# Optimization experiments

Measured on AMD Instinct MI355X. Metric: run time of the kernel, lower is better.

The kernel has to match this reference:

```python
import jax, jax.numpy as jnp
import numpy as np

D_MODEL = 1024
D_STATE = 16
BATCH = 16384
LN_EPS = 1e-5


def _linear_params(key, out_d, in_d):
    # torch nn.Linear default init: U(-1/sqrt(in_d), 1/sqrt(in_d))
    bound = 1.0 / np.sqrt(in_d)
    kw, kb = jax.random.split(key)
    W = jax.random.uniform(kw, (out_d, in_d), minval=-bound, maxval=bound, dtype=jnp.float32)
    b = jax.random.uniform(kb, (out_d,), minval=-bound, maxval=bound, dtype=jnp.float32)
    return W, b


def setup_inputs() -> dict:
    key = jax.random.key(0)
    k_x, k_b, k_c, k_dt, k_o = jax.random.split(key, 5)
    Wb, bb = _linear_params(k_b, D_STATE, D_MODEL)
    Wc, bc = _linear_params(k_c, D_STATE, D_MODEL)
    Wdt, bdt = _linear_params(k_dt, D_MODEL, D_MODEL)
    Wo, bo = _linear_params(k_o, D_MODEL, D_MODEL)
    return {
        "x": jax.random.normal(k_x, (BATCH, D_MODEL), dtype=jnp.float32),
        "gamma": jnp.ones((D_MODEL,), jnp.float32),   # LayerNorm weight
        "beta": jnp.zeros((D_MODEL,), jnp.float32),   # LayerNorm bias
        "Wb": Wb, "bb": bb,
        "Wc": Wc, "bc": bc,
        "Wdt": Wdt, "bdt": bdt,
        "D_skip": jnp.ones((D_MODEL,), jnp.float32),  # self.D parameter
        "Wo": Wo, "bo": bo,
    }


def reference(x, gamma, beta, Wb, bb, Wc, bc, Wdt, bdt, D_skip, Wo, bo):
    residual = x
    # LayerNorm
    mu = jnp.mean(x, axis=-1, keepdims=True)
    var = jnp.var(x, axis=-1, keepdims=True)
    xn = (x - mu) * jax.lax.rsqrt(var + LN_EPS) * gamma + beta  # (B, D)

    Bm = xn @ Wb.T + bb                     # (B, N)
    Cm = xn @ Wc.T + bc                     # (B, N)
    dt = jax.nn.softplus(xn @ Wdt.T + bdt)  # (B, D)
    # dA = exp(dt[...,None] * -exp(A_log)) is computed in the original but unused.

    # h = dt[:,:,None] * Bm[:,None,:] * xn[:,:,None]; y = (h * Cm[:,None,:]).sum(-1)
    # The N-reduction factors: sum_n Bm[b,n]*Cm[b,n] is d-independent.
    s = jnp.sum(Bm * Cm, axis=-1, keepdims=True)  # (B, 1)
    y = dt * xn * s + xn * D_skip                 # (B, D)

    y = y @ Wo.T + bo
    return y + residual  # dropout is identity at inference
```

## Files before the change

kernel.cpp:

```cpp
#include <hip/hip_runtime.h>
#include <math.h>

#define BATCH   16384
#define DMODEL  1024
#define NSTATE  16
#define LN_EPS  1e-5f

typedef __bf16 bf16x8 __attribute__((ext_vector_type(8)));
typedef float  f32x4  __attribute__((ext_vector_type(4)));

static __device__ __forceinline__ unsigned short f2bf(float v) {
  union { float f; unsigned u; } c; c.f = v;
  unsigned r = c.u + 0x7fffu + ((c.u >> 16) & 1u);
  return (unsigned short)(r >> 16);
}
static __device__ __forceinline__ float bf2f(unsigned short h) {
  union { unsigned u; float f; } c; c.u = ((unsigned)h) << 16;
  return c.f;
}

static __device__ __forceinline__ void gload16(const void* g, void* l) {
  __builtin_amdgcn_global_load_lds(
      (const __attribute__((address_space(1))) void*)g,
      (__attribute__((address_space(3))) void*)l, 16, 0, 0);
}

__global__ __launch_bounds__(256) void split_kernel(
    const float* __restrict__ src, unsigned short* __restrict__ hi,
    unsigned short* __restrict__ lo, int n) {
  int i = blockIdx.x * 256 + threadIdx.x;
  if (i < n) {
    float v = src[i];
    unsigned short h = f2bf(v);
    hi[i] = h;
    lo[i] = f2bf(v - bf2f(h));
  }
}

__global__ __launch_bounds__(256) void ln_kernel(
    const float* __restrict__ x, const float* __restrict__ gamma,
    const float* __restrict__ beta, unsigned short* __restrict__ xnh,
    unsigned short* __restrict__ xnl) {
  const int row = blockIdx.x;
  const int tid = threadIdx.x;
  const float4* xr = (const float4*)(x + (size_t)row * DMODEL);
  float4 v = xr[tid];
  float s = v.x + v.y + v.z + v.w;
  float q = v.x * v.x + v.y * v.y + v.z * v.z + v.w * v.w;
#pragma unroll
  for (int m = 1; m < 64; m <<= 1) {
    s += __shfl_xor(s, m, 64);
    q += __shfl_xor(q, m, 64);
  }
  __shared__ float ws[4], wq[4];
  int w = tid >> 6, l = tid & 63;
  if (l == 0) { ws[w] = s; wq[w] = q; }
  __syncthreads();
  s = ws[0] + ws[1] + ws[2] + ws[3];
  q = wq[0] + wq[1] + wq[2] + wq[3];
  float mu = s * (1.0f / DMODEL);
  float var = q * (1.0f / DMODEL) - mu * mu;
  float rs = rsqrtf(var + LN_EPS);
  float4 g = ((const float4*)gamma)[tid];
  float4 b = ((const float4*)beta)[tid];
  float xn[4];
  xn[0] = (v.x - mu) * rs * g.x + b.x;
  xn[1] = (v.y - mu) * rs * g.y + b.y;
  xn[2] = (v.z - mu) * rs * g.z + b.z;
  xn[3] = (v.w - mu) * rs * g.w + b.w;
  ushort4 hs, ls;
  unsigned short h;
  h = f2bf(xn[0]); hs.x = h; ls.x = f2bf(xn[0] - bf2f(h));
  h = f2bf(xn[1]); hs.y = h; ls.y = f2bf(xn[1] - bf2f(h));
  h = f2bf(xn[2]); hs.z = h; ls.z = f2bf(xn[2] - bf2f(h));
  h = f2bf(xn[3]); hs.w = h; ls.w = f2bf(xn[3] - bf2f(h));
  ((ushort4*)xnh)[(size_t)row * 256 + tid] = hs;
  ((ushort4*)xnl)[(size_t)row * 256 + tid] = ls;
}

template <int BM, int BN, int NBN, int WAVES_M, int WAVES_N, int MT, int NT, int EPI>
__global__ __launch_bounds__(WAVES_M * WAVES_N * 64) void gemm_kernel(
    const unsigned short* __restrict__ Ah_g, const unsigned short* __restrict__ Al_g,
    const unsigned short* __restrict__ Bh_g, const unsigned short* __restrict__ Bl_g,
    const float* __restrict__ e0,
    const float* __restrict__ e1,
    const float* __restrict__ e2,
    const unsigned short* __restrict__ e3h,
    const unsigned short* __restrict__ e3l,
    unsigned short* __restrict__ outh,
    unsigned short* __restrict__ outl,
    float* __restrict__ outf,
    int K) {
  constexpr int THREADS = WAVES_M * WAVES_N * 64;
  constexpr int GRID = (BATCH / BM) * NBN;
  static_assert(BM == WAVES_M * MT * 16 && BN == WAVES_N * NT * 16, "tile");

  __shared__ char smem[(BM + BN) * 256];
  char* sAh = smem;
  char* sAl = smem + BM * 128;
  char* sBh = smem + BM * 256;
  char* sBl = smem + BM * 256 + BN * 128;

  const int tid = threadIdx.x;
  const int l = tid & 63;
  const int w = tid >> 6;
  const int wm = w / WAVES_N;
  const int wn = w % WAVES_N;

  int bid = blockIdx.x;
  int sid = (bid & 7) * (GRID / 8) + (bid >> 3);
  const int bm = sid / NBN;
  const int bn = sid % NBN;
  const int m0 = bm * BM;
  const int n0 = bn * BN;

  f32x4 acc[MT][NT];
  const f32x4 fzero = {0.f, 0.f, 0.f, 0.f};
#pragma unroll
  for (int mi = 0; mi < MT; ++mi)
#pragma unroll
    for (int ni = 0; ni < NT; ++ni) acc[mi][ni] = fzero;

  constexpr int A_LOADS = (BM * 128) / (THREADS * 16);
  constexpr int B_LOADS = (BN * 128) / (THREADS * 16);

  for (int kt = 0; kt < K; kt += 64) {
#pragma unroll
    for (int i = 0; i < A_LOADS; ++i) {
      int q = i * THREADS + tid;
      int row = q >> 3;
      int c = (q & 7) ^ (row & 7);
      size_t goff = (size_t)(m0 + row) * K + kt + c * 8;
      int lbase = i * THREADS * 16 + w * 1024;
      gload16(Ah_g + goff, sAh + lbase);
      gload16(Al_g + goff, sAl + lbase);
    }
#pragma unroll
    for (int i = 0; i < B_LOADS; ++i) {
      int q = i * THREADS + tid;
      int row = q >> 3;
      int c = (q & 7) ^ (row & 7);
      size_t goff = (size_t)(n0 + row) * K + kt + c * 8;
      int lbase = i * THREADS * 16 + w * 1024;
      gload16(Bh_g + goff, sBh + lbase);
      gload16(Bl_g + goff, sBl + lbase);
    }
    __syncthreads();

#pragma unroll
    for (int kk = 0; kk < 2; ++kk) {
      bf16x8 ah[MT], al[MT], bh[NT], bl[NT];
#pragma unroll
      for (int mi = 0; mi < MT; ++mi) {
        int row = wm * MT * 16 + mi * 16 + (l & 15);
        int c = kk * 4 + (l >> 4);
        int off = row * 128 + ((c ^ (row & 7)) * 16);
        ah[mi] = *(const bf16x8*)(sAh + off);
        al[mi] = *(const bf16x8*)(sAl + off);
      }
#pragma unroll
      for (int ni = 0; ni < NT; ++ni) {
        int row = wn * NT * 16 + ni * 16 + (l & 15);
        int c = kk * 4 + (l >> 4);
        int off = row * 128 + ((c ^ (row & 7)) * 16);
        bh[ni] = *(const bf16x8*)(sBh + off);
        bl[ni] = *(const bf16x8*)(sBl + off);
      }
#pragma unroll
      for (int mi = 0; mi < MT; ++mi)
#pragma unroll
        for (int ni = 0; ni < NT; ++ni) {
          acc[mi][ni] = __builtin_amdgcn_mfma_f32_16x16x32_bf16(ah[mi], bh[ni], acc[mi][ni], 0, 0, 0);
          acc[mi][ni] = __builtin_amdgcn_mfma_f32_16x16x32_bf16(ah[mi], bl[ni], acc[mi][ni], 0, 0, 0);
          acc[mi][ni] = __builtin_amdgcn_mfma_f32_16x16x32_bf16(al[mi], bh[ni], acc[mi][ni], 0, 0, 0);
        }
    }
    __syncthreads();
  }

  if constexpr (EPI == 0) {
    int c = l & 15;
#pragma unroll
    for (int mi = 0; mi < MT; ++mi) {
#pragma unroll
      for (int j = 0; j < 4; ++j) {
        float bmv = acc[mi][0][j] + e0[c];
        float cmv = acc[mi][1][j] + e1[c];
        float p = bmv * cmv;
        p += __shfl_xor(p, 1, 64);
        p += __shfl_xor(p, 2, 64);
        p += __shfl_xor(p, 4, 64);
        p += __shfl_xor(p, 8, 64);
        if (c == 0) {
          int row = m0 + wm * MT * 16 + mi * 16 + (l >> 4) * 4 + j;
          outf[row] = p;
        }
      }
    }
  } else if constexpr (EPI == 1) {
#pragma unroll
    for (int mi = 0; mi < MT; ++mi) {
      int rbase = m0 + wm * MT * 16 + mi * 16 + (l >> 4) * 4;
#pragma unroll
      for (int ni = 0; ni < NT; ++ni) {
        int col = n0 + wn * NT * 16 + ni * 16 + (l & 15);
        float bdtc = e0[col];
        float dsk = e1[col];
#pragma unroll
        for (int j = 0; j < 4; ++j) {
          int row = rbase + j;
          size_t idx = (size_t)row * DMODEL + col;
          float v = acc[mi][ni][j] + bdtc;
          float sp = fmaxf(v, 0.0f) + __logf(1.0f + __expf(-fabsf(v)));
          float xnv = bf2f(e3h[idx]) + bf2f(e3l[idx]);
          float y = sp * xnv * e2[row] + xnv * dsk;
          unsigned short h = f2bf(y);
          outh[idx] = h;
          outl[idx] = f2bf(y - bf2f(h));
        }
      }
    }
  } else {
#pragma unroll
    for (int mi = 0; mi < MT; ++mi) {
      int rbase = m0 + wm * MT * 16 + mi * 16 + (l >> 4) * 4;
#pragma unroll
      for (int ni = 0; ni < NT; ++ni) {
        int col = n0 + wn * NT * 16 + ni * 16 + (l & 15);
        float bov = e0[col];
#pragma unroll
        for (int j = 0; j < 4; ++j) {
          int row = rbase + j;
          size_t idx = (size_t)row * DMODEL + col;
          outf[idx] = acc[mi][ni][j] + bov + e1[idx];
        }
      }
    }
  }
}

extern "C" void kernel_launch(void* const* d_in, const int* in_sizes, int n_in,
                              void* d_out, int out_size, void* d_ws, size_t ws_size,
                              hipStream_t stream) {
  const float* x = (const float*)d_in[0];
  const float* gamma = (const float*)d_in[1];
  const float* beta = (const float*)d_in[2];
  const float* Wb = (const float*)d_in[3];
  const float* bb = (const float*)d_in[4];
  const float* Wc = (const float*)d_in[5];
  const float* bc = (const float*)d_in[6];
  const float* Wdt = (const float*)d_in[7];
  const float* bdt = (const float*)d_in[8];
  const float* Dsk = (const float*)d_in[9];
  const float* Wo = (const float*)d_in[10];
  const float* bo = (const float*)d_in[11];
  float* out = (float*)d_out;

  char* ws = (char*)d_ws;
  size_t off = 0;
  auto alloc = [&](size_t bytes) {
    char* p = ws + off;
    off = (off + bytes + 255) & ~(size_t)255;
    return p;
  };
  unsigned short* XNH = (unsigned short*)alloc((size_t)BATCH * DMODEL * 2);
  unsigned short* XNL = (unsigned short*)alloc((size_t)BATCH * DMODEL * 2);
  unsigned short* YH  = (unsigned short*)alloc((size_t)BATCH * DMODEL * 2);
  unsigned short* YL  = (unsigned short*)alloc((size_t)BATCH * DMODEL * 2);
  unsigned short* WDTH = (unsigned short*)alloc((size_t)DMODEL * DMODEL * 2);
  unsigned short* WDTL = (unsigned short*)alloc((size_t)DMODEL * DMODEL * 2);
  unsigned short* WOH  = (unsigned short*)alloc((size_t)DMODEL * DMODEL * 2);
  unsigned short* WOL  = (unsigned short*)alloc((size_t)DMODEL * DMODEL * 2);
  unsigned short* WBCH = (unsigned short*)alloc((size_t)2 * NSTATE * DMODEL * 2);
  unsigned short* WBCL = (unsigned short*)alloc((size_t)2 * NSTATE * DMODEL * 2);
  float* S = (float*)alloc((size_t)BATCH * 4);

  split_kernel<<<(DMODEL * DMODEL) / 256, 256, 0, stream>>>(Wdt, WDTH, WDTL, DMODEL * DMODEL);
  split_kernel<<<(DMODEL * DMODEL) / 256, 256, 0, stream>>>(Wo, WOH, WOL, DMODEL * DMODEL);
  split_kernel<<<(NSTATE * DMODEL) / 256, 256, 0, stream>>>(Wb, WBCH, WBCL, NSTATE * DMODEL);
  split_kernel<<<(NSTATE * DMODEL) / 256, 256, 0, stream>>>(
      Wc, WBCH + NSTATE * DMODEL, WBCL + NSTATE * DMODEL, NSTATE * DMODEL);

  ln_kernel<<<BATCH, 256, 0, stream>>>(x, gamma, beta, XNH, XNL);

  gemm_kernel<128, 32, 1, 4, 1, 2, 2, 0><<<BATCH / 128, 256, 0, stream>>>(
      XNH, XNL, WBCH, WBCL, bb, bc, nullptr, nullptr, nullptr, nullptr, nullptr, S, DMODEL);

  gemm_kernel<128, 128, 8, 2, 2, 4, 4, 1><<<(BATCH / 128) * 8, 256, 0, stream>>>(
      XNH, XNL, WDTH, WDTL, bdt, Dsk, S, XNH, XNL, YH, YL, nullptr, DMODEL);

  gemm_kernel<128, 128, 8, 2, 2, 4, 4, 2><<<(BATCH / 128) * 8, 256, 0, stream>>>(
      YH, YL, WOH, WOL, bo, x, nullptr, nullptr, nullptr, nullptr, nullptr, out, DMODEL);
}
```

Measured before the change: 366.5 us.

## Pack hi/lo bf16 splits along K and use double-buffered 256x256 GEMM

Stores the hi and lo bf16 halves interleaved per row (K=2048 physical) so the three-product split GEMM becomes a single K=3072 GEMM over packed operands. The main GEMMs move to 256x256 tiles with 8 waves, double-buffered LDS staging through direct global-to-LDS loads, explicit waitcnt/barrier scheduling and setprio around the MFMA blocks. The weight split kernels are merged into one pack kernel, and a dedicated small kernel computes the B·C row sums. This is meant to raise MFMA utilisation and hide load latency, at the cost of 128KB LDS per block, one block per CU, and fragile hand-written synchronisation.

```diff
diff --git a/kernel.cpp b/kernel.cpp
--- a/kernel.cpp
+++ b/kernel.cpp
@@ -3,7 +3,8 @@
 
 #define BATCH   16384
 #define DMODEL  1024
-#define NSTATE  16
+#define KPACK   3072
+#define KPHYS   2048
 #define LN_EPS  1e-5f
 
 typedef __bf16 bf16x8 __attribute__((ext_vector_type(8)));
@@ -25,22 +26,38 @@
       (__attribute__((address_space(3))) void*)l, 16, 0, 0);
 }
 
-__global__ __launch_bounds__(256) void split_kernel(
-    const float* __restrict__ src, unsigned short* __restrict__ hi,
-    unsigned short* __restrict__ lo, int n) {
-  int i = blockIdx.x * 256 + threadIdx.x;
-  if (i < n) {
-    float v = src[i];
-    unsigned short h = f2bf(v);
-    hi[i] = h;
-    lo[i] = f2bf(v - bf2f(h));
-  }
+#define S_BAR() __builtin_amdgcn_s_barrier()
+#define LGKM0() do { asm volatile("s_waitcnt lgkmcnt(0)" ::: "memory"); \
+                     __builtin_amdgcn_sched_barrier(0); } while (0)
+#define VMC8()  do { asm volatile("s_waitcnt vmcnt(8)" ::: "memory"); \
+                     __builtin_amdgcn_sched_barrier(0); } while (0)
+
+__global__ __launch_bounds__(256) void pack_kernel(
+    const float* __restrict__ Wdt, const float* __restrict__ Wo,
+    const float* __restrict__ Wb, const float* __restrict__ Wc,
+    unsigned short* __restrict__ WdtP, unsigned short* __restrict__ WoP,
+    unsigned short* __restrict__ WbcP) {
+  int r = blockIdx.x;
+  const float* src;
+  unsigned short* dst;
+  if (r < 1024)      { src = Wdt + (size_t)r * 1024;        dst = WdtP + (size_t)r * KPHYS; }
+  else if (r < 2048) { src = Wo  + (size_t)(r-1024) * 1024; dst = WoP  + (size_t)(r-1024) * KPHYS; }
+  else if (r < 2064) { src = Wb  + (size_t)(r-2048) * 1024; dst = WbcP + (size_t)(r-2048) * KPHYS; }
+  else               { src = Wc  + (size_t)(r-2064) * 1024; dst = WbcP + (size_t)(r-2064+16) * KPHYS; }
+  int t = threadIdx.x;
+  float4 v = ((const float4*)src)[t];
+  ushort4 hs, ls; unsigned short h;
+  h = f2bf(v.x); hs.x = h; ls.x = f2bf(v.x - bf2f(h));
+  h = f2bf(v.y); hs.y = h; ls.y = f2bf(v.y - bf2f(h));
+  h = f2bf(v.z); hs.z = h; ls.z = f2bf(v.z - bf2f(h));
+  h = f2bf(v.w); hs.w = h; ls.w = f2bf(v.w - bf2f(h));
+  ((ushort4*)dst)[t] = hs;
+  ((ushort4*)(dst + 1024))[t] = ls;
 }
 
 __global__ __launch_bounds__(256) void ln_kernel(
     const float* __restrict__ x, const float* __restrict__ gamma,
-    const float* __restrict__ beta, unsigned short* __restrict__ xnh,
-    unsigned short* __restrict__ xnl) {
+    const float* __restrict__ beta, unsigned short* __restrict__ xnp) {
   const int row = blockIdx.x;
   const int tid = threadIdx.x;
   const float4* xr = (const float4*)(x + (size_t)row * DMODEL);
@@ -63,176 +80,217 @@
   float rs = rsqrtf(var + LN_EPS);
   float4 g = ((const float4*)gamma)[tid];
   float4 b = ((const float4*)beta)[tid];
-  float xn[4];
-  xn[0] = (v.x - mu) * rs * g.x + b.x;
-  xn[1] = (v.y - mu) * rs * g.y + b.y;
-  xn[2] = (v.z - mu) * rs * g.z + b.z;
-  xn[3] = (v.w - mu) * rs * g.w + b.w;
-  ushort4 hs, ls;
-  unsigned short h;
-  h = f2bf(xn[0]); hs.x = h; ls.x = f2bf(xn[0] - bf2f(h));
-  h = f2bf(xn[1]); hs.y = h; ls.y = f2bf(xn[1] - bf2f(h));
-  h = f2bf(xn[2]); hs.z = h; ls.z = f2bf(xn[2] - bf2f(h));
-  h = f2bf(xn[3]); hs.w = h; ls.w = f2bf(xn[3] - bf2f(h));
-  ((ushort4*)xnh)[(size_t)row * 256 + tid] = hs;
-  ((ushort4*)xnl)[(size_t)row * 256 + tid] = ls;
-}
-
-template <int BM, int BN, int NBN, int WAVES_M, int WAVES_N, int MT, int NT, int EPI>
-__global__ __launch_bounds__(WAVES_M * WAVES_N * 64) void gemm_kernel(
-    const unsigned short* __restrict__ Ah_g, const unsigned short* __restrict__ Al_g,
-    const unsigned short* __restrict__ Bh_g, const unsigned short* __restrict__ Bl_g,
-    const float* __restrict__ e0,
-    const float* __restrict__ e1,
-    const float* __restrict__ e2,
-    const unsigned short* __restrict__ e3h,
-    const unsigned short* __restrict__ e3l,
-    unsigned short* __restrict__ outh,
-    unsigned short* __restrict__ outl,
-    float* __restrict__ outf,
-    int K) {
-  constexpr int THREADS = WAVES_M * WAVES_N * 64;
-  constexpr int GRID = (BATCH / BM) * NBN;
-  static_assert(BM == WAVES_M * MT * 16 && BN == WAVES_N * NT * 16, "tile");
-
-  __shared__ char smem[(BM + BN) * 256];
-  char* sAh = smem;
-  char* sAl = smem + BM * 128;
-  char* sBh = smem + BM * 256;
-  char* sBl = smem + BM * 256 + BN * 128;
-
+  float xn0 = (v.x - mu) * rs * g.x + b.x;
+  float xn1 = (v.y - mu) * rs * g.y + b.y;
+  float xn2 = (v.z - mu) * rs * g.z + b.z;
+  float xn3 = (v.w - mu) * rs * g.w + b.w;
+  ushort4 hs, ls; unsigned short h;
+  h = f2bf(xn0); hs.x = h; ls.x = f2bf(xn0 - bf2f(h));
+  h = f2bf(xn1); hs.y = h; ls.y = f2bf(xn1 - bf2f(h));
+  h = f2bf(xn2); hs.z = h; ls.z = f2bf(xn2 - bf2f(h));
+  h = f2bf(xn3); hs.w = h; ls.w = f2bf(xn3 - bf2f(h));
+  unsigned short* dst = xnp + (size_t)row * KPHYS;
+  ((ushort4*)dst)[tid] = hs;
+  ((ushort4*)(dst + 1024))[tid] = ls;
+}
+
+__global__ __launch_bounds__(256) void bc_kernel(
+    const unsigned short* __restrict__ XNP, const unsigned short* __restrict__ WbcP,
+    const float* __restrict__ bb, const float* __restrict__ bcv, float* __restrict__ S) {
+  __shared__ char smem[(64 + 32) * 128];
+  char* sA = smem;
+  char* sB = smem + 64 * 128;
   const int tid = threadIdx.x;
   const int l = tid & 63;
   const int w = tid >> 6;
-  const int wm = w / WAVES_N;
-  const int wn = w % WAVES_N;
-
-  int bid = blockIdx.x;
-  int sid = (bid & 7) * (GRID / 8) + (bid >> 3);
-  const int bm = sid / NBN;
-  const int bn = sid % NBN;
-  const int m0 = bm * BM;
-  const int n0 = bn * BN;
-
-  f32x4 acc[MT][NT];
-  const f32x4 fzero = {0.f, 0.f, 0.f, 0.f};
-#pragma unroll
-  for (int mi = 0; mi < MT; ++mi)
-#pragma unroll
-    for (int ni = 0; ni < NT; ++ni) acc[mi][ni] = fzero;
-
-  constexpr int A_LOADS = (BM * 128) / (THREADS * 16);
-  constexpr int B_LOADS = (BN * 128) / (THREADS * 16);
-
-  for (int kt = 0; kt < K; kt += 64) {
-#pragma unroll
-    for (int i = 0; i < A_LOADS; ++i) {
-      int q = i * THREADS + tid;
-      int row = q >> 3;
-      int c = (q & 7) ^ (row & 7);
-      size_t goff = (size_t)(m0 + row) * K + kt + c * 8;
-      int lbase = i * THREADS * 16 + w * 1024;
-      gload16(Ah_g + goff, sAh + lbase);
-      gload16(Al_g + goff, sAl + lbase);
-    }
-#pragma unroll
-    for (int i = 0; i < B_LOADS; ++i) {
-      int q = i * THREADS + tid;
-      int row = q >> 3;
-      int c = (q & 7) ^ (row & 7);
-      size_t goff = (size_t)(n0 + row) * K + kt + c * 8;
-      int lbase = i * THREADS * 16 + w * 1024;
-      gload16(Bh_g + goff, sBh + lbase);
-      gload16(Bl_g + goff, sBl + lbase);
+  const int m0 = blockIdx.x * 64;
+  f32x4 acc0 = {0.f, 0.f, 0.f, 0.f};
+  f32x4 acc1 = {0.f, 0.f, 0.f, 0.f};
+  for (int kt = 0; kt < KPACK; kt += 64) {
+    int ksA = kt < 2048 ? kt : kt - 2048;
+    int ksB = kt < 1024 ? kt : kt - 1024;
+#pragma unroll
+    for (int i = 0; i < 2; ++i) {
+      int qq = i * 256 + tid;
+      int row = qq >> 3, ch = qq & 7;
+      gload16(XNP + (size_t)(m0 + row) * KPHYS + ksA + ((ch ^ (row & 7)) << 3),
+              sA + (i * 256 + w * 64) * 16);
+    }
+    {
+      int row = tid >> 3, ch = tid & 7;
+      gload16(WbcP + (size_t)row * KPHYS + ksB + ((ch ^ (row & 7)) << 3),
+              sB + (w * 64) * 16);
     }
     __syncthreads();
-
 #pragma unroll
     for (int kk = 0; kk < 2; ++kk) {
-      bf16x8 ah[MT], al[MT], bh[NT], bl[NT];
-#pragma unroll
-      for (int mi = 0; mi < MT; ++mi) {
-        int row = wm * MT * 16 + mi * 16 + (l & 15);
-        int c = kk * 4 + (l >> 4);
-        int off = row * 128 + ((c ^ (row & 7)) * 16);
-        ah[mi] = *(const bf16x8*)(sAh + off);
-        al[mi] = *(const bf16x8*)(sAl + off);
-      }
-#pragma unroll
-      for (int ni = 0; ni < NT; ++ni) {
-        int row = wn * NT * 16 + ni * 16 + (l & 15);
-        int c = kk * 4 + (l >> 4);
-        int off = row * 128 + ((c ^ (row & 7)) * 16);
-        bh[ni] = *(const bf16x8*)(sBh + off);
-        bl[ni] = *(const bf16x8*)(sBl + off);
-      }
-#pragma unroll
-      for (int mi = 0; mi < MT; ++mi)
-#pragma unroll
-        for (int ni = 0; ni < NT; ++ni) {
-          acc[mi][ni] = __builtin_amdgcn_mfma_f32_16x16x32_bf16(ah[mi], bh[ni], acc[mi][ni], 0, 0, 0);
-          acc[mi][ni] = __builtin_amdgcn_mfma_f32_16x16x32_bf16(ah[mi], bl[ni], acc[mi][ni], 0, 0, 0);
-          acc[mi][ni] = __builtin_amdgcn_mfma_f32_16x16x32_bf16(al[mi], bh[ni], acc[mi][ni], 0, 0, 0);
-        }
+      int cs = ((kk * 4 + (l >> 4)) ^ (l & 7)) * 16;
+      bf16x8 a  = *(const bf16x8*)(sA + (w * 16 + (l & 15)) * 128 + cs);
+      bf16x8 b0 = *(const bf16x8*)(sB + ((l & 15)) * 128 + cs);
+      bf16x8 b1 = *(const bf16x8*)(sB + (16 + (l & 15)) * 128 + cs);
+      acc0 = __builtin_amdgcn_mfma_f32_16x16x32_bf16(a, b0, acc0, 0, 0, 0);
+      acc1 = __builtin_amdgcn_mfma_f32_16x16x32_bf16(a, b1, acc1, 0, 0, 0);
     }
     __syncthreads();
   }
-
-  if constexpr (EPI == 0) {
-    int c = l & 15;
-#pragma unroll
-    for (int mi = 0; mi < MT; ++mi) {
+  int c = l & 15;
+#pragma unroll
+  for (int j = 0; j < 4; ++j) {
+    float bmv = acc0[j] + bb[c];
+    float cmv = acc1[j] + bcv[c];
+    float p = bmv * cmv;
+    p += __shfl_xor(p, 1, 64);
+    p += __shfl_xor(p, 2, 64);
+    p += __shfl_xor(p, 4, 64);
+    p += __shfl_xor(p, 8, 64);
+    if (c == 0) S[m0 + w * 16 + (l >> 4) * 4 + j] = p;
+  }
+}
+
+template <int EPI>
+__global__ __launch_bounds__(512, 2) void gemm8_kernel(
+    const unsigned short* __restrict__ Ag,
+    const unsigned short* __restrict__ Bg,
+    const float* __restrict__ e0,
+    const float* __restrict__ e1,
+    const float* __restrict__ S,
+    unsigned short* __restrict__ YP,
+    float* __restrict__ outf) {
+  __shared__ char smem[131072];
+  char* const bufA[2] = { smem, smem + 65536 };
+  char* const bufB[2] = { smem + 32768, smem + 98304 };
+
+  const int tid = threadIdx.x;
+  const int l = tid & 63;
+  const int w = tid >> 6;
+  const int wm = w >> 2;
+  const int wn = w & 3;
+
+  const int bid = blockIdx.x;
+  const int sid = (bid & 7) * 32 + (bid >> 3);
+  const int m0 = (sid >> 2) * 256;
+  const int n0 = (sid & 3) * 256;
+
+  f32x4 acc[8][4];
+#pragma unroll
+  for (int a = 0; a < 8; ++a)
+#pragma unroll
+    for (int b = 0; b < 4; ++b) acc[a][b] = (f32x4){0.f, 0.f, 0.f, 0.f};
+
+  auto STAGE = [&](int bufi, int kt) {
+    const int ksA = kt < 2048 ? kt : kt - 2048;
+    const int ksB = kt < 1024 ? kt : kt - 1024;
+#pragma unroll
+    for (int r = 0; r < 4; ++r) {
+      int qq = r * 512 + tid;
+      int row = qq >> 3, ch = qq & 7;
+      gload16(Ag + (size_t)(m0 + row) * KPHYS + ksA + ((ch ^ (row & 7)) << 3),
+              bufA[bufi] + (r * 512 + w * 64) * 16);
+    }
+#pragma unroll
+    for (int r = 0; r < 4; ++r) {
+      int qq = r * 512 + tid;
+      int row = qq >> 3, ch = qq & 7;
+      gload16(Bg + (size_t)(n0 + row) * KPHYS + ksB + ((ch ^ (row & 7)) << 3),
+              bufB[bufi] + (r * 512 + w * 64) * 16);
+    }
+  };
+
+  const int rbA = (wm * 128 + (l & 15)) * 128;
+  const int rbB = (wn * 64 + (l & 15)) * 128;
+  int cs[2];
+  cs[0] = (((l >> 4)) ^ (l & 7)) * 16;
+  cs[1] = ((4 + (l >> 4)) ^ (l & 7)) * 16;
+
+  bf16x8 aF[4][2], bF[2][2][2];
+  auto LDA = [&](int bufi, int qm) {
+#pragma unroll
+    for (int mi = 0; mi < 4; ++mi)
+#pragma unroll
+      for (int kk = 0; kk < 2; ++kk)
+        aF[mi][kk] = *(const bf16x8*)(bufA[bufi] + rbA + qm * 8192 + mi * 2048 + cs[kk]);
+  };
+  auto LDB = [&](int bufi, int qn) {
+#pragma unroll
+    for (int ni = 0; ni < 2; ++ni)
+#pragma unroll
+      for (int kk = 0; kk < 2; ++kk)
+        bF[qn][ni][kk] = *(const bf16x8*)(bufB[bufi] + rbB + qn * 4096 + ni * 2048 + cs[kk]);
+  };
+  auto MFMA = [&](int qm, int qn) {
+    __builtin_amdgcn_s_setprio(1);
+#pragma unroll
+    for (int kk = 0; kk < 2; ++kk)
+#pragma unroll
+      for (int mi = 0; mi < 4; ++mi)
+#pragma unroll
+        for (int ni = 0; ni < 2; ++ni)
+          acc[qm * 4 + mi][qn * 2 + ni] = __builtin_amdgcn_mfma_f32_16x16x32_bf16(
+              aF[mi][kk], bF[qn][ni][kk], acc[qm * 4 + mi][qn * 2 + ni], 0, 0, 0);
+    __builtin_amdgcn_s_setprio(0);
+  };
+
+  STAGE(0, 0);
+  STAGE(1, 64);
+  VMC8();
+  S_BAR();
+
+  for (int it = 0; it < 24; ++it) {
+    const int ktA = it * 128;
+    const int kt2 = (ktA + 128 <= KPACK - 64) ? ktA + 128 : KPACK - 64;
+    const int kt3 = (ktA + 192 <= KPACK - 64) ? ktA + 192 : KPACK - 64;
+    LDA(0, 0); LDB(0, 0);
+    S_BAR(); LGKM0(); MFMA(0, 0); S_BAR();
+    LDB(0, 1);
+    S_BAR(); LGKM0(); MFMA(0, 1); S_BAR();
+    LDA(0, 1);
+    S_BAR(); LGKM0(); MFMA(1, 1); S_BAR();
+    STAGE(0, kt2);
+    S_BAR(); MFMA(1, 0); VMC8(); S_BAR();
+    LDA(1, 0); LDB(1, 0);
+    S_BAR(); LGKM0(); MFMA(0, 0); S_BAR();
+    LDB(1, 1);
+    S_BAR(); LGKM0(); MFMA(0, 1); S_BAR();
+    LDA(1, 1);
+    S_BAR(); LGKM0(); MFMA(1, 1); S_BAR();
+    STAGE(1, kt3);
+    S_BAR(); MFMA(1, 0); VMC8(); S_BAR();
+  }
+
+  if constexpr (EPI == 1) {
+#pragma unroll
+    for (int a = 0; a < 8; ++a) {
+      int rw = m0 + wm * 128 + (a >> 2) * 64 + (a & 3) * 16 + (l >> 4) * 4;
 #pragma unroll
       for (int j = 0; j < 4; ++j) {
-        float bmv = acc[mi][0][j] + e0[c];
-        float cmv = acc[mi][1][j] + e1[c];
-        float p = bmv * cmv;
-        p += __shfl_xor(p, 1, 64);
-        p += __shfl_xor(p, 2, 64);
-        p += __shfl_xor(p, 4, 64);
-        p += __shfl_xor(p, 8, 64);
-        if (c == 0) {
-          int row = m0 + wm * MT * 16 + mi * 16 + (l >> 4) * 4 + j;
-          outf[row] = p;
+        int r = rw + j;
+        float sv = S[r];
+        size_t base = (size_t)r * KPHYS;
+#pragma unroll
+        for (int b = 0; b < 4; ++b) {
+          int col = n0 + wn * 64 + (b >> 1) * 32 + (b & 1) * 16 + (l & 15);
+          float v = acc[a][b][j] + e0[col];
+          float sp = fmaxf(v, 0.f) + __logf(1.f + __expf(-fabsf(v)));
+          float xnv = bf2f(Ag[base + col]) + bf2f(Ag[base + 1024 + col]);
+          float y = sp * xnv * sv + xnv * e1[col];
+          unsigned short h = f2bf(y);
+          YP[base + col] = h;
+          YP[base + 1024 + col] = f2bf(y - bf2f(h));
         }
       }
     }
-  } else if constexpr (EPI == 1) {
-#pragma unroll
-    for (int mi = 0; mi < MT; ++mi) {
-      int rbase = m0 + wm * MT * 16 + mi * 16 + (l >> 4) * 4;
-#pragma unroll
-      for (int ni = 0; ni < NT; ++ni) {
-        int col = n0 + wn * NT * 16 + ni * 16 + (l & 15);
-        float bdtc = e0[col];
-        float dsk = e1[col];
-#pragma unroll
-        for (int j = 0; j < 4; ++j) {
-          int row = rbase + j;
-          size_t idx = (size_t)row * DMODEL + col;
-          float v = acc[mi][ni][j] + bdtc;
-          float sp = fmaxf(v, 0.0f) + __logf(1.0f + __expf(-fabsf(v)));
-          float xnv = bf2f(e3h[idx]) + bf2f(e3l[idx]);
-          float y = sp * xnv * e2[row] + xnv * dsk;
-          unsigned short h = f2bf(y);
-          outh[idx] = h;
-          outl[idx] = f2bf(y - bf2f(h));
-        }
-      }
-    }
   } else {
 #pragma unroll
-    for (int mi = 0; mi < MT; ++mi) {
-      int rbase = m0 + wm * MT * 16 + mi * 16 + (l >> 4) * 4;
-#pragma unroll
-      for (int ni = 0; ni < NT; ++ni) {
-        int col = n0 + wn * NT * 16 + ni * 16 + (l & 15);
-        float bov = e0[col];
-#pragma unroll
-        for (int j = 0; j < 4; ++j) {
-          int row = rbase + j;
-          size_t idx = (size_t)row * DMODEL + col;
-          outf[idx] = acc[mi][ni][j] + bov + e1[idx];
+    for (int a = 0; a < 8; ++a) {
+      int rw = m0 + wm * 128 + (a >> 2) * 64 + (a & 3) * 16 + (l >> 4) * 4;
+#pragma unroll
+      for (int j = 0; j < 4; ++j) {
+        int r = rw + j;
+        size_t base = (size_t)r * DMODEL;
+#pragma unroll
+        for (int b = 0; b < 4; ++b) {
+          int col = n0 + wn * 64 + (b >> 1) * 32 + (b & 1) * 16 + (l & 15);
+          outf[base + col] = acc[a][b][j] + e0[col] + e1[base + col];
         }
       }
     }
@@ -263,32 +321,16 @@
     off = (off + bytes + 255) & ~(size_t)255;
     return p;
   };
-  unsigned short* XNH = (unsigned short*)alloc((size_t)BATCH * DMODEL * 2);
-  unsigned short* XNL = (unsigned short*)alloc((size_t)BATCH * DMODEL * 2);
-  unsigned short* YH  = (unsigned short*)alloc((size_t)BATCH * DMODEL * 2);
-  unsigned short* YL  = (unsigned short*)alloc((size_t)BATCH * DMODEL * 2);
-  unsigned short* WDTH = (unsigned short*)alloc((size_t)DMODEL * DMODEL * 2);
-  unsigned short* WDTL = (unsigned short*)alloc((size_t)DMODEL * DMODEL * 2);
-  unsigned short* WOH  = (unsigned short*)alloc((size_t)DMODEL * DMODEL * 2);
-  unsigned short* WOL  = (unsigned short*)alloc((size_t)DMODEL * DMODEL * 2);
-  unsigned short* WBCH = (unsigned short*)alloc((size_t)2 * NSTATE * DMODEL * 2);
-  unsigned short* WBCL = (unsigned short*)alloc((size_t)2 * NSTATE * DMODEL * 2);
+  unsigned short* XNP  = (unsigned short*)alloc((size_t)BATCH * KPHYS * 2);
+  unsigned short* YP   = (unsigned short*)alloc((size_t)BATCH * KPHYS * 2);
+  unsigned short* WdtP = (unsigned short*)alloc((size_t)DMODEL * KPHYS * 2);
+  unsigned short* WoP  = (unsigned short*)alloc((size_t)DMODEL * KPHYS * 2);
+  unsigned short* WbcP = (unsigned short*)alloc((size_t)32 * KPHYS * 2);
   float* S = (float*)alloc((size_t)BATCH * 4);
 
-  split_kernel<<<(DMODEL * DMODEL) / 256, 256, 0, stream>>>(Wdt, WDTH, WDTL, DMODEL * DMODEL);
-  split_kernel<<<(DMODEL * DMODEL) / 256, 256, 0, stream>>>(Wo, WOH, WOL, DMODEL * DMODEL);
-  split_kernel<<<(NSTATE * DMODEL) / 256, 256, 0, stream>>>(Wb, WBCH, WBCL, NSTATE * DMODEL);
-  split_kernel<<<(NSTATE * DMODEL) / 256, 256, 0, stream>>>(
-      Wc, WBCH + NSTATE * DMODEL, WBCL + NSTATE * DMODEL, NSTATE * DMODEL);
-
-  ln_kernel<<<BATCH, 256, 0, stream>>>(x, gamma, beta, XNH, XNL);
-
-  gemm_kernel<128, 32, 1, 4, 1, 2, 2, 0><<<BATCH / 128, 256, 0, stream>>>(
-      XNH, XNL, WBCH, WBCL, bb, bc, nullptr, nullptr, nullptr, nullptr, nullptr, S, DMODEL);
-
-  gemm_kernel<128, 128, 8, 2, 2, 4, 4, 1><<<(BATCH / 128) * 8, 256, 0, stream>>>(
-      XNH, XNL, WDTH, WDTL, bdt, Dsk, S, XNH, XNL, YH, YL, nullptr, DMODEL);
-
-  gemm_kernel<128, 128, 8, 2, 2, 4, 4, 2><<<(BATCH / 128) * 8, 256, 0, stream>>>(
-      YH, YL, WOH, WOL, bo, x, nullptr, nullptr, nullptr, nullptr, nullptr, out, DMODEL);
-}
+  pack_kernel<<<2080, 256, 0, stream>>>(Wdt, Wo, Wb, Wc, WdtP, WoP, WbcP);
+  ln_kernel<<<BATCH, 256, 0, stream>>>(x, gamma, beta, XNP);
+  bc_kernel<<<BATCH / 64, 256, 0, stream>>>(XNP, WbcP, bb, bc, S);
+  gemm8_kernel<1><<<256, 512, 0, stream>>>(XNP, WdtP, bdt, Dsk, S, YP, nullptr);
+  gemm8_kernel<2><<<256, 512, 0, stream>>>(YP, WoP, bo, x, nullptr, nullptr, out);
+}
```

Result: slower. 384.6 us (+4.9%).
